# Optimization experiments

Measured on AMD Instinct MI355X. Metric: run time of the kernel, lower is better.

The kernel has to match this reference:

```python
import jax, jax.numpy as jnp
from jax import lax
import numpy as np

CHANNEL_N = 16
EMB = 128
B, H, W = 16, 256, 256


def setup_inputs() -> dict:
    key = jax.random.key(0)
    ks = jax.random.split(key, 8)
    x = jax.random.uniform(ks[0], (B, CHANNEL_N, H, W), dtype=jnp.float32)
    fire_mask = (jax.random.uniform(ks[1], (B, 1, H, W)) < 0.5).astype(jnp.float32)
    s = 0.05
    w1 = jax.random.normal(ks[2], (3 * CHANNEL_N, EMB), dtype=jnp.float32) * s
    b1 = jnp.zeros((EMB,), jnp.float32)
    w2 = jax.random.normal(ks[3], (EMB, EMB), dtype=jnp.float32) * s
    b2 = jnp.zeros((EMB,), jnp.float32)
    w3 = jax.random.normal(ks[4], (EMB, CHANNEL_N), dtype=jnp.float32) * s
    b3 = jnp.zeros((CHANNEL_N,), jnp.float32)
    return {"x": x, "fire_mask": fire_mask, "w1": w1, "b1": b1, "w2": w2, "b2": b2, "w3": w3, "b3": b3}


def _forward(x, fire_mask, w1, b1, w2, b2, w3, b3):
    # depthwise Sobel conv (torch conv2d = cross-correlation, same as lax default)
    sob = jnp.array([[-1., 0., 1.], [-2., 0., 2.], [-1., 0., 1.]], jnp.float32)
    kx = jnp.tile(sob[None, None], (CHANNEL_N, 1, 1, 1))   # OIHW, groups=16
    ky = jnp.tile(sob.T[None, None], (CHANNEL_N, 1, 1, 1))
    conv = lambda k: lax.conv_general_dilated(x, k, (1, 1), 'SAME', feature_group_count=CHANNEL_N)
    feats = jnp.concatenate([x, conv(kx), conv(ky)], axis=1)  # [B,48,H,W]

    # alive mask: 3x3 max-pool of alpha channel > 0.1
    alpha = x[:, 3:4]
    pooled = lax.reduce_window(alpha, -jnp.inf, lax.max, (1, 1, 3, 3), (1, 1, 1, 1), 'SAME')
    alive = (pooled > 0.1).astype(x.dtype)
    combined = fire_mask * alive                     # [B,1,H,W]
    # nonzero-indexing semantics: update written wherever combined != 0
    sel = (combined != 0).astype(x.dtype)

    f = feats.transpose(0, 2, 3, 1)                  # [B,H,W,48]
    h = jax.nn.relu(f @ w1 + b1)
    h = jax.nn.relu(h @ w2 + b2)
    u = h @ w3 + b3                                  # [B,H,W,16]
    updates = u * sel.transpose(0, 2, 3, 1)          # zero outside selected cells
    return updates.transpose(0, 3, 1, 2)             # [B,16,H,W]


def reference(x, fire_mask, w1, b1, w2, b2, w3, b3):
    return _forward(x, fire_mask, w1, b1, w2, b2, w3, b3)
```

## Files before the change

### kernel.cpp

```cpp
#include <hip/hip_runtime.h>


using bf16x8 = __attribute__((ext_vector_type(8))) __bf16;
using f32x4  = __attribute__((ext_vector_type(4))) float;

__device__ __forceinline__ unsigned f2bf(float f) {
    unsigned u = __float_as_uint(f);
    u += 0x7fffu + ((u >> 16) & 1u);
    return u >> 16;
}

#define WS1_OFF 0
#define WS2_OFF 8192
#define WS3_OFF 24576

__global__ __launch_bounds__(256)
void prep_weights(const float* __restrict__ w1, const float* __restrict__ b1,
                  const float* __restrict__ w2, const float* __restrict__ w3,
                  unsigned short* __restrict__ ws) {
    const int gid = blockIdx.x * 256 + threadIdx.x;
    if (gid < 1024) {
        const int s = gid;
        const int mt = s >> 7, kb = (s >> 6) & 1, lane = s & 63;
        const int q = lane >> 4, ln = lane & 15;
#pragma unroll
        for (int j = 0; j < 8; ++j) {
            const int k = kb * 32 + q * 8 + j;
            float val = 0.f;
            if (k < 48) { const int c = k / 3, t = k - 3 * c; val = w1[(t * 16 + c) * 128 + mt * 16 + ln]; }
            else if (k == 48) val = b1[mt * 16 + ln];
            ws[WS1_OFF + s * 8 + j] = (unsigned short)f2bf(val);
        }
    } else if (gid < 3072) {
        const int s2 = gid - 1024;
        const int mt = s2 >> 8, kb = (s2 >> 6) & 3, lane = s2 & 63;
        const int q = lane >> 4, ln = lane & 15;
#pragma unroll
        for (int j = 0; j < 8; ++j) {
            const int k = kb * 32 + q * 8 + j;
            ws[WS2_OFF + s2 * 8 + j] = (unsigned short)f2bf(w2[k * 128 + mt * 16 + ln]);
        }
    } else if (gid < 3328) {
        const int s3 = gid - 3072;
        const int kb = s3 >> 6, lane = s3 & 63;
        const int q = lane >> 4, ln = lane & 15;
#pragma unroll
        for (int j = 0; j < 8; ++j) {
            const int k = kb * 32 + q * 8 + j;
            ws[WS3_OFF + s3 * 8 + j] = (unsigned short)f2bf(w3[k * 16 + ln]);
        }
    }
}


#define SM_XS    0
#define SM_W2    65536
#define SM_WR    98304
#define SM_AUX   155648
#define SM_B2L   159744
#define SM_B3L   160256
#define SM_TOTAL 160320

#define GLDS16(gp, lp) __builtin_amdgcn_global_load_lds(                     \
    (const __attribute__((address_space(1))) void*)(gp),                     \
    (__attribute__((address_space(3))) void*)(lp), 16, 0, 0)

#define STAGE_UNIT(chv, rowv) do {                                           \
        const int _sl = (rowv) & 3;                                          \
        char* _ld = smem + SM_XS + (size_t)(((_sl) * 16 + (chv)) * 256) * 4; \
        if ((unsigned)(rowv) < 256u) {                                       \
            const float* _gs = xb + ((size_t)(chv) << 16)                    \
                             + (size_t)(unsigned)(rowv) * 256 + lane * 4;    \
            GLDS16(_gs, _ld);                                                \
        } else {                                                             \
            *(float4*)(_ld + lane * 16) = make_float4(0.f, 0.f, 0.f, 0.f);   \
        } } while (0)

#define HCH(j) ((((j) ^ (ln & 7)) << 4))

extern "C" __global__ __launch_bounds__(512)
void fused_kernel(const float* __restrict__ x, const float* __restrict__ fmask,
                  const unsigned short* __restrict__ wf,
                  const float* __restrict__ b2, const float* __restrict__ b3,
                  float* __restrict__ out) {
    extern __shared__ char smem[];
    float (*xs)[16][256] = (float (*)[16][256])(smem + SM_XS);
    char* W2L = smem + SM_W2;

    const int t = threadIdx.x;
    const int wv = t >> 6, lane = t & 63;
    const int q = lane >> 4, ln = lane & 15;
    const int rhalf = t >> 8;
    const int col = t & 255;
    char* region = smem + SM_WR + wv * 7168;

    const int bb = blockIdx.x >> 5;
    const int h0 = (blockIdx.x & 31) << 3;
    const float* xb = x + ((size_t)bb << 20);

    {
        const uint4* s1 = (const uint4*)(wf + WS1_OFF);
        uint4* dW = (uint4*)W2L;
        dW[t]       = s1[t];
        dW[t + 512] = s1[t + 512];
        if (t < 256) ((uint4*)(smem + SM_AUX))[t] = ((const uint4*)(wf + WS3_OFF))[t];
        if (t < 128) ((float*)(smem + SM_B2L))[t] = b2[t];
        if (t < 16)  ((float*)(smem + SM_B3L))[t] = b3[t];
    }
    __syncthreads();
    bf16x8 W1f[8][2];
#pragma unroll
    for (int mt = 0; mt < 8; ++mt) {
        W1f[mt][0] = *(const bf16x8*)(W2L + ((mt * 2 + 0) * 64 + lane) * 16);
        W1f[mt][1] = *(const bf16x8*)(W2L + ((mt * 2 + 1) * 64 + lane) * 16);
    }
    __syncthreads();
    {
        const uint4* s2 = (const uint4*)(wf + WS2_OFF);
        uint4* dW = (uint4*)W2L;
#pragma unroll
        for (int i2 = 0; i2 < 4; ++i2) dW[t + i2 * 512] = s2[t + i2 * 512];
    }

    const int cL = (col > 0)   ? col - 1 : 0;
    const int cR = (col < 255) ? col + 1 : 255;
    const float mL = (col > 0)   ? 1.f : 0.f;
    const float mR = (col < 255) ? 1.f : 0.f;

#pragma unroll
    for (int k = 0; k < 8; ++k) {
        const int u = wv + 8 * k;
        STAGE_UNIT(u >> 2, h0 - 1 + (u & 3));
    }

    for (int i = 0; i < 4; ++i) {
        const int r0 = h0 + 2 * i;
        const int r  = r0 + rhalf;
        __syncthreads();
        const float fv = fmask[((size_t)bb << 16) + (size_t)r * 256 + col];

        const int sT = (r - 1) & 3, sC = r & 3, sB = (r + 1) & 3;
        char* fb = region + lane * 112;
        unsigned pk[24];
        unsigned carry = 0;
#pragma unroll
        for (int c = 0; c < 16; ++c) {
            const float* rT = xs[sT][c];
            const float* rC = xs[sC][c];
            const float* rB = xs[sB][c];
            const float v00 = rT[cL] * mL, v01 = rT[col], v02 = rT[cR] * mR;
            const float v10 = rC[cL] * mL, v11 = rC[col], v12 = rC[cR] * mR;
            const float v20 = rB[cL] * mL, v21 = rB[col], v22 = rB[cR] * mR;
            const float sx = (v02 + 2.f * v12 + v22) - (v00 + 2.f * v10 + v20);
            const float sy = (v20 + 2.f * v21 + v22) - (v00 + 2.f * v01 + v02);
            if (c == 3) {
                float mx = fmaxf(fmaxf(fmaxf(v00, v01), fmaxf(v02, v10)),
                                 fmaxf(fmaxf(v11, v12), fmaxf(fmaxf(v20, v21), v22)));
                const float selv = (mx > 0.1f) ? 1.f : 0.f;
                *(float*)(fb + 96) = (fv != 0.f) ? selv : 0.f;
            }
            const unsigned ux = f2bf(v11), usx = f2bf(sx), usy = f2bf(sy);
            if ((c & 1) == 0) { pk[(c >> 1) * 3] = ux | (usx << 16); carry = usy; }
            else { pk[(c >> 1) * 3 + 1] = carry | (ux << 16);
                   pk[(c >> 1) * 3 + 2] = usx | (usy << 16); }
            if (c == 2)  *(uint4*)(fb +  0) = make_uint4(pk[0],  pk[1],  pk[2],  pk[3]);
            if (c == 5)  *(uint4*)(fb + 16) = make_uint4(pk[4],  pk[5],  pk[6],  pk[7]);
            if (c == 8)  *(uint4*)(fb + 32) = make_uint4(pk[8],  pk[9],  pk[10], pk[11]);
            if (c == 10) *(uint4*)(fb + 48) = make_uint4(pk[12], pk[13], pk[14], pk[15]);
            if (c == 13) *(uint4*)(fb + 64) = make_uint4(pk[16], pk[17], pk[18], pk[19]);
            if (c == 15) *(uint4*)(fb + 80) = make_uint4(pk[20], pk[21], pk[22], pk[23]);
        }
        __syncthreads();
        if (i < 3) {
#pragma unroll
            for (int k = 0; k < 4; ++k) {
                const int u = wv + 8 * k;
                STAGE_UNIT(u >> 1, r0 + 3 + (u & 1));
            }
        }

#pragma unroll
        for (int p = 0; p < 2; ++p) {
            char* Hb = region + p * 3584;
            bf16x8 Bk0a[2], Bk1a[2];
            float sva[2];
#pragma unroll
            for (int s2 = 0; s2 < 2; ++s2) {
                const int s = p * 2 + s2;
                const char* fp = region + (s * 16 + ln) * 112;
                Bk0a[s2] = *(const bf16x8*)(fp + q * 16);
                bf16x8 t1 = {};
                if (q < 2)       t1 = *(const bf16x8*)(fp + (4 + q) * 16);
                else if (q == 2) t1[0] = (__bf16)1.0f;
                Bk1a[s2] = t1;
                sva[s2] = *(const float*)(fp + 96);
            }
            f32x4 a3h;
#pragma unroll
            for (int s2 = 0; s2 < 2; ++s2) {
                bf16x8 B2[4];
                __builtin_amdgcn_s_setprio(1);
#pragma unroll
                for (int m = 0; m < 4; ++m) {
                    f32x4 a = {};
                    a = __builtin_amdgcn_mfma_f32_16x16x32_bf16(W1f[m][0], Bk0a[s2], a, 0, 0, 0);
                    a = __builtin_amdgcn_mfma_f32_16x16x32_bf16(W1f[m][1], Bk1a[s2], a, 0, 0, 0);
                    const unsigned r01 = f2bf(fmaxf(a[0], 0.f)) | (f2bf(fmaxf(a[1], 0.f)) << 16);
                    const unsigned r23 = f2bf(fmaxf(a[2], 0.f)) | (f2bf(fmaxf(a[3], 0.f)) << 16);
                    *(uint2*)(Hb + ln * 128 + HCH(m * 2 + (q >> 1)) + ((q & 1) << 3))
                        = make_uint2(r01, r23);
                }
                __builtin_amdgcn_s_setprio(0);
                B2[0] = *(const bf16x8*)(Hb + ln * 128 + HCH(q));
                B2[1] = *(const bf16x8*)(Hb + ln * 128 + HCH(4 + q));
                __builtin_amdgcn_s_setprio(1);
#pragma unroll
                for (int m = 4; m < 8; ++m) {
                    f32x4 a = {};
                    a = __builtin_amdgcn_mfma_f32_16x16x32_bf16(W1f[m][0], Bk0a[s2], a, 0, 0, 0);
                    a = __builtin_amdgcn_mfma_f32_16x16x32_bf16(W1f[m][1], Bk1a[s2], a, 0, 0, 0);
                    const unsigned r01 = f2bf(fmaxf(a[0], 0.f)) | (f2bf(fmaxf(a[1], 0.f)) << 16);
                    const unsigned r23 = f2bf(fmaxf(a[2], 0.f)) | (f2bf(fmaxf(a[3], 0.f)) << 16);
                    *(uint2*)(Hb + ln * 128 + HCH((m - 4) * 2 + (q >> 1)) + ((q & 1) << 3))
                        = make_uint2(r01, r23);
                }
                __builtin_amdgcn_s_setprio(0);
                B2[2] = *(const bf16x8*)(Hb + ln * 128 + HCH(q));
                B2[3] = *(const bf16x8*)(Hb + ln * 128 + HCH(4 + q));
                bf16x8 B3[4];
                __builtin_amdgcn_s_setprio(1);
#pragma unroll
                for (int m = 0; m < 4; ++m) {
                    f32x4 a = *(const f32x4*)(smem + SM_B2L + m * 64 + q * 16);
#pragma unroll
                    for (int kb = 0; kb < 4; ++kb) {
                        const bf16x8 Af = *(const bf16x8*)(W2L + ((m * 4 + kb) * 64 + lane) * 16);
                        a = __builtin_amdgcn_mfma_f32_16x16x32_bf16(Af, B2[kb], a, 0, 0, 0);
                    }
                    const unsigned r01 = f2bf(fmaxf(a[0], 0.f)) | (f2bf(fmaxf(a[1], 0.f)) << 16);
                    const unsigned r23 = f2bf(fmaxf(a[2], 0.f)) | (f2bf(fmaxf(a[3], 0.f)) << 16);
                    *(uint2*)(Hb + ln * 128 + HCH(m * 2 + (q >> 1)) + ((q & 1) << 3))
                        = make_uint2(r01, r23);
                }
                __builtin_amdgcn_s_setprio(0);
                B3[0] = *(const bf16x8*)(Hb + ln * 128 + HCH(q));
                B3[1] = *(const bf16x8*)(Hb + ln * 128 + HCH(4 + q));
                __builtin_amdgcn_s_setprio(1);
#pragma unroll
                for (int m = 4; m < 8; ++m) {
                    f32x4 a = *(const f32x4*)(smem + SM_B2L + m * 64 + q * 16);
#pragma unroll
                    for (int kb = 0; kb < 4; ++kb) {
                        const bf16x8 Af = *(const bf16x8*)(W2L + ((m * 4 + kb) * 64 + lane) * 16);
                        a = __builtin_amdgcn_mfma_f32_16x16x32_bf16(Af, B2[kb], a, 0, 0, 0);
                    }
                    const unsigned r01 = f2bf(fmaxf(a[0], 0.f)) | (f2bf(fmaxf(a[1], 0.f)) << 16);
                    const unsigned r23 = f2bf(fmaxf(a[2], 0.f)) | (f2bf(fmaxf(a[3], 0.f)) << 16);
                    *(uint2*)(Hb + ln * 128 + HCH((m - 4) * 2 + (q >> 1)) + ((q & 1) << 3))
                        = make_uint2(r01, r23);
                }
                __builtin_amdgcn_s_setprio(0);
                B3[2] = *(const bf16x8*)(Hb + ln * 128 + HCH(q));
                B3[3] = *(const bf16x8*)(Hb + ln * 128 + HCH(4 + q));
                f32x4 a3 = *(const f32x4*)(smem + SM_B3L + q * 16);
                __builtin_amdgcn_s_setprio(1);
#pragma unroll
                for (int kb = 0; kb < 4; ++kb) {
                    const bf16x8 W3a = *(const bf16x8*)(smem + SM_AUX + (kb * 64 + lane) * 16);
                    a3 = __builtin_amdgcn_mfma_f32_16x16x32_bf16(W3a, B3[kb], a3, 0, 0, 0);
                }
                __builtin_amdgcn_s_setprio(0);
                const float svv = sva[s2];
#pragma unroll
                for (int r4 = 0; r4 < 4; ++r4) a3[r4] *= svv;
                if (s2 == 0) a3h = a3;
                else {
#pragma unroll
                    for (int r4 = 0; r4 < 4; ++r4) {
                        *(float*)(Hb + (q * 4 + r4) * 132 + ln * 4)      = a3h[r4];
                        *(float*)(Hb + (q * 4 + r4) * 132 + 64 + ln * 4) = a3[r4];
                    }
                }
            }
        }
        {
            float* orow = out + (((size_t)(bb * 16)) << 16) + (size_t)r * 256
                        + (wv & 3) * 64 + lane;
#pragma unroll
            for (int ch = 0; ch < 16; ++ch) {
                const float v = *(const float*)(region + (lane >> 5) * 3584
                              + ch * 132 + ((lane >> 4) & 1) * 64 + (lane & 15) * 4);
                orow[(size_t)ch << 16] = v;
            }
        }
    }
}

extern "C" void kernel_launch(void* const* d_in, const int* in_sizes, int n_in,
                              void* d_out, int out_size, void* d_ws, size_t ws_size,
                              hipStream_t stream) {
    (void)in_sizes; (void)n_in; (void)out_size; (void)ws_size;
    const float* x  = (const float*)d_in[0];
    const float* fm = (const float*)d_in[1];
    const float* w1 = (const float*)d_in[2];
    const float* b1 = (const float*)d_in[3];
    const float* w2 = (const float*)d_in[4];
    const float* b2 = (const float*)d_in[5];
    const float* w3 = (const float*)d_in[6];
    const float* b3 = (const float*)d_in[7];
    float* o = (float*)d_out;
    unsigned short* ws = (unsigned short*)d_ws;

    prep_weights<<<dim3(13), dim3(256), 0, stream>>>(w1, b1, w2, w3, ws);

    static bool s_attr_done = false;
    if (!s_attr_done) {
        hipFuncSetAttribute((const void*)fused_kernel,
                            hipFuncAttributeMaxDynamicSharedMemorySize, SM_TOTAL);
        s_attr_done = true;
    }
    fused_kernel<<<dim3(512), dim3(512), SM_TOTAL, stream>>>(x, fm, ws, b2, b3, o);
}
```

Baseline: 220.9 us.

## Widen hidden tile to full 128 rows, hoist B loads, per-pair output bounce

The hidden-activation buffer is widened from two 64-column halves to one 256-byte row per pixel, so each MLP layer runs 8 m-tiles in one pass with 4 B-fragment loads instead of two half passes. Feature fragments for all four pixel groups are loaded once before the pair loop. Output is staged through a small padded bounce buffer and stored after each pair rather than once at the end. Float-to-bf16 packing now uses the hardware __bf16 conversion, and the Sobel loop is regrouped by channel pairs, at some cost in register pressure.

```diff
diff --git a/kernel.cpp b/kernel.cpp
--- a/kernel.cpp
+++ b/kernel.cpp
@@ -8,6 +8,12 @@
     unsigned u = __float_as_uint(f);
     u += 0x7fffu + ((u >> 16) & 1u);
     return u >> 16;
+}
+
+__device__ __forceinline__ unsigned pack2bf(float lo, float hi) {
+    unsigned short a = __builtin_bit_cast(unsigned short, (__bf16)lo);
+    unsigned short b = __builtin_bit_cast(unsigned short, (__bf16)hi);
+    return (unsigned)a | ((unsigned)b << 16);
 }
 
 #define WS1_OFF 0
@@ -93,6 +99,8 @@
     const int rhalf = t >> 8;
     const int col = t & 255;
     char* region = smem + SM_WR + wv * 7168;
+    char* H = region;
+    float* bounce = (float*)(region + 4096);
 
     const int bb = blockIdx.x >> 5;
     const int h0 = (blockIdx.x & 31) << 3;
@@ -142,33 +150,37 @@
         const int sT = (r - 1) & 3, sC = r & 3, sB = (r + 1) & 3;
         char* fb = region + lane * 112;
         unsigned pk[24];
-        unsigned carry = 0;
-#pragma unroll
-        for (int c = 0; c < 16; ++c) {
-            const float* rT = xs[sT][c];
-            const float* rC = xs[sC][c];
-            const float* rB = xs[sB][c];
-            const float v00 = rT[cL] * mL, v01 = rT[col], v02 = rT[cR] * mR;
-            const float v10 = rC[cL] * mL, v11 = rC[col], v12 = rC[cR] * mR;
-            const float v20 = rB[cL] * mL, v21 = rB[col], v22 = rB[cR] * mR;
-            const float sx = (v02 + 2.f * v12 + v22) - (v00 + 2.f * v10 + v20);
-            const float sy = (v20 + 2.f * v21 + v22) - (v00 + 2.f * v01 + v02);
-            if (c == 3) {
-                float mx = fmaxf(fmaxf(fmaxf(v00, v01), fmaxf(v02, v10)),
-                                 fmaxf(fmaxf(v11, v12), fmaxf(fmaxf(v20, v21), v22)));
-                const float selv = (mx > 0.1f) ? 1.f : 0.f;
-                *(float*)(fb + 96) = (fv != 0.f) ? selv : 0.f;
+#pragma unroll
+        for (int g = 0; g < 8; ++g) {
+            float va[2], sxa[2], sya[2];
+#pragma unroll
+            for (int h = 0; h < 2; ++h) {
+                const int c = 2 * g + h;
+                const float* rT = xs[sT][c];
+                const float* rC = xs[sC][c];
+                const float* rB = xs[sB][c];
+                const float v00 = rT[cL] * mL, v01 = rT[col], v02 = rT[cR] * mR;
+                const float v10 = rC[cL] * mL, v11 = rC[col], v12 = rC[cR] * mR;
+                const float v20 = rB[cL] * mL, v21 = rB[col], v22 = rB[cR] * mR;
+                sxa[h] = (v02 + 2.f * v12 + v22) - (v00 + 2.f * v10 + v20);
+                sya[h] = (v20 + 2.f * v21 + v22) - (v00 + 2.f * v01 + v02);
+                va[h] = v11;
+                if (g == 1 && h == 1) {
+                    float mx = fmaxf(fmaxf(fmaxf(v00, v01), fmaxf(v02, v10)),
+                                     fmaxf(fmaxf(v11, v12), fmaxf(fmaxf(v20, v21), v22)));
+                    const float selv = (mx > 0.1f) ? 1.f : 0.f;
+                    *(float*)(fb + 96) = (fv != 0.f) ? selv : 0.f;
+                }
             }
-            const unsigned ux = f2bf(v11), usx = f2bf(sx), usy = f2bf(sy);
-            if ((c & 1) == 0) { pk[(c >> 1) * 3] = ux | (usx << 16); carry = usy; }
-            else { pk[(c >> 1) * 3 + 1] = carry | (ux << 16);
-                   pk[(c >> 1) * 3 + 2] = usx | (usy << 16); }
-            if (c == 2)  *(uint4*)(fb +  0) = make_uint4(pk[0],  pk[1],  pk[2],  pk[3]);
-            if (c == 5)  *(uint4*)(fb + 16) = make_uint4(pk[4],  pk[5],  pk[6],  pk[7]);
-            if (c == 8)  *(uint4*)(fb + 32) = make_uint4(pk[8],  pk[9],  pk[10], pk[11]);
-            if (c == 10) *(uint4*)(fb + 48) = make_uint4(pk[12], pk[13], pk[14], pk[15]);
-            if (c == 13) *(uint4*)(fb + 64) = make_uint4(pk[16], pk[17], pk[18], pk[19]);
-            if (c == 15) *(uint4*)(fb + 80) = make_uint4(pk[20], pk[21], pk[22], pk[23]);
+            pk[g * 3 + 0] = pack2bf(va[0],  sxa[0]);
+            pk[g * 3 + 1] = pack2bf(sya[0], va[1]);
+            pk[g * 3 + 2] = pack2bf(sxa[1], sya[1]);
+            if (g == 1) *(uint4*)(fb +  0) = make_uint4(pk[0],  pk[1],  pk[2],  pk[3]);
+            if (g == 3) { *(uint4*)(fb + 16) = make_uint4(pk[4],  pk[5],  pk[6],  pk[7]);
+                          *(uint4*)(fb + 32) = make_uint4(pk[8],  pk[9],  pk[10], pk[11]); }
+            if (g == 5) *(uint4*)(fb + 48) = make_uint4(pk[12], pk[13], pk[14], pk[15]);
+            if (g == 6) *(uint4*)(fb + 64) = make_uint4(pk[16], pk[17], pk[18], pk[19]);
+            if (g == 7) *(uint4*)(fb + 80) = make_uint4(pk[20], pk[21], pk[22], pk[23]);
         }
         __syncthreads();
         if (i < 3) {
@@ -179,89 +191,60 @@
             }
         }
 
+        bf16x8 Bk0[4], Bk1[4];
+        float sv[4];
+#pragma unroll
+        for (int s = 0; s < 4; ++s) {
+            const char* fp = region + (s * 16 + ln) * 112;
+            Bk0[s] = *(const bf16x8*)(fp + q * 16);
+            bf16x8 t1 = {};
+            if (q < 2)       t1 = *(const bf16x8*)(fp + (4 + q) * 16);
+            else if (q == 2) t1[0] = (__bf16)1.0f;
+            Bk1[s] = t1;
+            sv[s] = *(const float*)(fp + 96);
+        }
+
 #pragma unroll
         for (int p = 0; p < 2; ++p) {
-            char* Hb = region + p * 3584;
-            bf16x8 Bk0a[2], Bk1a[2];
-            float sva[2];
+            f32x4 a3h;
 #pragma unroll
             for (int s2 = 0; s2 < 2; ++s2) {
-                const int s = p * 2 + s2;
-                const char* fp = region + (s * 16 + ln) * 112;
-                Bk0a[s2] = *(const bf16x8*)(fp + q * 16);
-                bf16x8 t1 = {};
-                if (q < 2)       t1 = *(const bf16x8*)(fp + (4 + q) * 16);
-                else if (q == 2) t1[0] = (__bf16)1.0f;
-                Bk1a[s2] = t1;
-                sva[s2] = *(const float*)(fp + 96);
-            }
-            f32x4 a3h;
-#pragma unroll
-            for (int s2 = 0; s2 < 2; ++s2) {
+                const int s = 2 * p + s2;
+                __builtin_amdgcn_s_setprio(1);
+#pragma unroll
+                for (int mt = 0; mt < 8; ++mt) {
+                    f32x4 a = {};
+                    a = __builtin_amdgcn_mfma_f32_16x16x32_bf16(W1f[mt][0], Bk0[s], a, 0, 0, 0);
+                    a = __builtin_amdgcn_mfma_f32_16x16x32_bf16(W1f[mt][1], Bk1[s], a, 0, 0, 0);
+                    const unsigned r01 = pack2bf(fmaxf(a[0], 0.f), fmaxf(a[1], 0.f));
+                    const unsigned r23 = pack2bf(fmaxf(a[2], 0.f), fmaxf(a[3], 0.f));
+                    *(uint2*)(H + ln * 256 + HCH(mt * 2 + (q >> 1)) + ((q & 1) << 3))
+                        = make_uint2(r01, r23);
+                }
+                __builtin_amdgcn_s_setprio(0);
                 bf16x8 B2[4];
+#pragma unroll
+                for (int kb = 0; kb < 4; ++kb)
+                    B2[kb] = *(const bf16x8*)(H + ln * 256 + HCH(kb * 4 + q));
                 __builtin_amdgcn_s_setprio(1);
 #pragma unroll
-                for (int m = 0; m < 4; ++m) {
-                    f32x4 a = {};
-                    a = __builtin_amdgcn_mfma_f32_16x16x32_bf16(W1f[m][0], Bk0a[s2], a, 0, 0, 0);
-                    a = __builtin_amdgcn_mfma_f32_16x16x32_bf16(W1f[m][1], Bk1a[s2], a, 0, 0, 0);
-                    const unsigned r01 = f2bf(fmaxf(a[0], 0.f)) | (f2bf(fmaxf(a[1], 0.f)) << 16);
-                    const unsigned r23 = f2bf(fmaxf(a[2], 0.f)) | (f2bf(fmaxf(a[3], 0.f)) << 16);
-                    *(uint2*)(Hb + ln * 128 + HCH(m * 2 + (q >> 1)) + ((q & 1) << 3))
-                        = make_uint2(r01, r23);
-                }
-                __builtin_amdgcn_s_setprio(0);
-                B2[0] = *(const bf16x8*)(Hb + ln * 128 + HCH(q));
-                B2[1] = *(const bf16x8*)(Hb + ln * 128 + HCH(4 + q));
-                __builtin_amdgcn_s_setprio(1);
-#pragma unroll
-                for (int m = 4; m < 8; ++m) {
-                    f32x4 a = {};
-                    a = __builtin_amdgcn_mfma_f32_16x16x32_bf16(W1f[m][0], Bk0a[s2], a, 0, 0, 0);
-                    a = __builtin_amdgcn_mfma_f32_16x16x32_bf16(W1f[m][1], Bk1a[s2], a, 0, 0, 0);
-                    const unsigned r01 = f2bf(fmaxf(a[0], 0.f)) | (f2bf(fmaxf(a[1], 0.f)) << 16);
-                    const unsigned r23 = f2bf(fmaxf(a[2], 0.f)) | (f2bf(fmaxf(a[3], 0.f)) << 16);
-                    *(uint2*)(Hb + ln * 128 + HCH((m - 4) * 2 + (q >> 1)) + ((q & 1) << 3))
-                        = make_uint2(r01, r23);
-                }
-                __builtin_amdgcn_s_setprio(0);
-                B2[2] = *(const bf16x8*)(Hb + ln * 128 + HCH(q));
-                B2[3] = *(const bf16x8*)(Hb + ln * 128 + HCH(4 + q));
-                bf16x8 B3[4];
-                __builtin_amdgcn_s_setprio(1);
-#pragma unroll
-                for (int m = 0; m < 4; ++m) {
-                    f32x4 a = *(const f32x4*)(smem + SM_B2L + m * 64 + q * 16);
+                for (int mt = 0; mt < 8; ++mt) {
+                    f32x4 a = *(const f32x4*)(smem + SM_B2L + mt * 64 + q * 16);
 #pragma unroll
                     for (int kb = 0; kb < 4; ++kb) {
-                        const bf16x8 Af = *(const bf16x8*)(W2L + ((m * 4 + kb) * 64 + lane) * 16);
+                        const bf16x8 Af = *(const bf16x8*)(W2L + ((mt * 4 + kb) * 64 + lane) * 16);
                         a = __builtin_amdgcn_mfma_f32_16x16x32_bf16(Af, B2[kb], a, 0, 0, 0);
                     }
-                    const unsigned r01 = f2bf(fmaxf(a[0], 0.f)) | (f2bf(fmaxf(a[1], 0.f)) << 16);
-                    const unsigned r23 = f2bf(fmaxf(a[2], 0.f)) | (f2bf(fmaxf(a[3], 0.f)) << 16);
-                    *(uint2*)(Hb + ln * 128 + HCH(m * 2 + (q >> 1)) + ((q & 1) << 3))
+                    const unsigned r01 = pack2bf(fmaxf(a[0], 0.f), fmaxf(a[1], 0.f));
+                    const unsigned r23 = pack2bf(fmaxf(a[2], 0.f), fmaxf(a[3], 0.f));
+                    *(uint2*)(H + ln * 256 + HCH(mt * 2 + (q >> 1)) + ((q & 1) << 3))
                         = make_uint2(r01, r23);
                 }
                 __builtin_amdgcn_s_setprio(0);
-                B3[0] = *(const bf16x8*)(Hb + ln * 128 + HCH(q));
-                B3[1] = *(const bf16x8*)(Hb + ln * 128 + HCH(4 + q));
-                __builtin_amdgcn_s_setprio(1);
-#pragma unroll
-                for (int m = 4; m < 8; ++m) {
-                    f32x4 a = *(const f32x4*)(smem + SM_B2L + m * 64 + q * 16);
-#pragma unroll
-                    for (int kb = 0; kb < 4; ++kb) {
-                        const bf16x8 Af = *(const bf16x8*)(W2L + ((m * 4 + kb) * 64 + lane) * 16);
-                        a = __builtin_amdgcn_mfma_f32_16x16x32_bf16(Af, B2[kb], a, 0, 0, 0);
-                    }
-                    const unsigned r01 = f2bf(fmaxf(a[0], 0.f)) | (f2bf(fmaxf(a[1], 0.f)) << 16);
-                    const unsigned r23 = f2bf(fmaxf(a[2], 0.f)) | (f2bf(fmaxf(a[3], 0.f)) << 16);
-                    *(uint2*)(Hb + ln * 128 + HCH((m - 4) * 2 + (q >> 1)) + ((q & 1) << 3))
-                        = make_uint2(r01, r23);
-                }
-                __builtin_amdgcn_s_setprio(0);
-                B3[2] = *(const bf16x8*)(Hb + ln * 128 + HCH(q));
-                B3[3] = *(const bf16x8*)(Hb + ln * 128 + HCH(4 + q));
+                bf16x8 B3[4];
+#pragma unroll
+                for (int kb = 0; kb < 4; ++kb)
+                    B3[kb] = *(const bf16x8*)(H + ln * 256 + HCH(kb * 4 + q));
                 f32x4 a3 = *(const f32x4*)(smem + SM_B3L + q * 16);
                 __builtin_amdgcn_s_setprio(1);
 #pragma unroll
@@ -270,27 +253,28 @@
                     a3 = __builtin_amdgcn_mfma_f32_16x16x32_bf16(W3a, B3[kb], a3, 0, 0, 0);
                 }
                 __builtin_amdgcn_s_setprio(0);
-                const float svv = sva[s2];
+                const float svv = sv[s];
 #pragma unroll
                 for (int r4 = 0; r4 < 4; ++r4) a3[r4] *= svv;
                 if (s2 == 0) a3h = a3;
                 else {
 #pragma unroll
                     for (int r4 = 0; r4 < 4; ++r4) {
-                        *(float*)(Hb + (q * 4 + r4) * 132 + ln * 4)      = a3h[r4];
-                        *(float*)(Hb + (q * 4 + r4) * 132 + 64 + ln * 4) = a3[r4];
+                        bounce[(q * 4 + r4) * 33 + ln]      = a3h[r4];
+                        bounce[(q * 4 + r4) * 33 + 16 + ln] = a3[r4];
                     }
                 }
             }
-        }
-        {
-            float* orow = out + (((size_t)(bb * 16)) << 16) + (size_t)r * 256
-                        + (wv & 3) * 64 + lane;
-#pragma unroll
-            for (int ch = 0; ch < 16; ++ch) {
-                const float v = *(const float*)(region + (lane >> 5) * 3584
-                              + ch * 132 + ((lane >> 4) & 1) * 64 + (lane & 15) * 4);
-                orow[(size_t)ch << 16] = v;
+            {
+                const int px32 = lane & 31;
+                const int chb  = lane >> 5;
+                float* orow = out + (((size_t)(bb * 16)) << 16) + (size_t)r * 256
+                            + (wv & 3) * 64 + p * 32 + px32;
+#pragma unroll
+                for (int i8 = 0; i8 < 8; ++i8) {
+                    const int ch = chb + 2 * i8;
+                    orow[(size_t)ch << 16] = bounce[ch * 33 + px32];
+                }
             }
         }
     }
```

Result: faster. 210.9 us (-4.5%).
